# Kernel optimization log

Hardware: AMD Instinct MI355X
Metric: run time of the kernel (lower is better)

Reference implementation:

```python
import jax, jax.numpy as jnp
import numpy as np

D_MODEL = 1024
N_HEADS = 16
HEAD_DIM = D_MODEL // N_HEADS
N_MEM = 16
EPS = 1e-5
ROPE_THETA = 10000.0


def layernorm(x, g, b):
    mu = jnp.mean(x, axis=-1, keepdims=True)
    var = jnp.mean(jnp.square(x - mu), axis=-1, keepdims=True)
    return (x - mu) * jax.lax.rsqrt(var + EPS) * g + b


def rope_cos_sin(seq_len, head_dim, dtype):
    inv_freq = 1.0 / (ROPE_THETA ** (jnp.arange(0, head_dim, 2, dtype=jnp.float32) / head_dim))
    pos = jnp.arange(seq_len, dtype=jnp.float32)
    freqs = pos[:, None] * inv_freq[None, :]            # [S, hd/2]
    emb = jnp.concatenate([freqs, freqs], axis=-1)       # [S, hd]
    return jnp.cos(emb).astype(dtype), jnp.sin(emb).astype(dtype)


def rotate_half(x):
    x1, x2 = jnp.split(x, 2, axis=-1)
    return jnp.concatenate([-x2, x1], axis=-1)


def setup_inputs() -> dict:
    key = jax.random.key(0)
    ks = jax.random.split(key, 8)
    B, T, D = 2, 2048, D_MODEL
    x = jax.random.normal(ks[0], (B, T, D), dtype=jnp.float32)
    memory_tokens = jax.random.normal(ks[1], (1, N_MEM, D), dtype=jnp.float32) * 0.02
    s = 1.0 / np.sqrt(D)
    qkv_w = jax.random.uniform(ks[2], (3 * D, D), minval=-s, maxval=s, dtype=jnp.float32)
    qkv_b = jax.random.uniform(ks[3], (3 * D,), minval=-s, maxval=s, dtype=jnp.float32)
    out_w = jax.random.uniform(ks[4], (D, D), minval=-s, maxval=s, dtype=jnp.float32)
    out_b = jax.random.uniform(ks[5], (D,), minval=-s, maxval=s, dtype=jnp.float32)
    norm_g = jnp.ones((D,), jnp.float32)
    norm_b = jnp.zeros((D,), jnp.float32)
    normm_g = jnp.ones((D,), jnp.float32)
    normm_b = jnp.zeros((D,), jnp.float32)
    return {"x": x, "memory_tokens": memory_tokens, "qkv_w": qkv_w, "qkv_b": qkv_b,
            "out_w": out_w, "out_b": out_b, "norm_g": norm_g, "norm_b": norm_b,
            "normm_g": normm_g, "normm_b": normm_b}


def reference(x, memory_tokens, qkv_w, qkv_b, out_w, out_b, norm_g, norm_b, normm_g, normm_b):
    B, T, D = x.shape
    S = N_MEM + T
    residual = x
    x_norm = layernorm(x, norm_g, norm_b)
    mem = layernorm(jnp.broadcast_to(memory_tokens, (B, N_MEM, D)), normm_g, normm_b)
    xm = jnp.concatenate([mem, x_norm], axis=1)                # [B, S, D]
    qkv = xm @ qkv_w.T + qkv_b                                 # [B, S, 3D]
    qkv = qkv.reshape(B, S, 3, N_HEADS, HEAD_DIM)
    q = jnp.transpose(qkv[:, :, 0], (0, 2, 1, 3))              # [B, H, S, hd]
    k = jnp.transpose(qkv[:, :, 1], (0, 2, 1, 3))
    v = jnp.transpose(qkv[:, :, 2], (0, 2, 1, 3))
    cos, sin = rope_cos_sin(S, HEAD_DIM, x.dtype)              # [S, hd]
    q = q * cos + rotate_half(q) * sin
    k = k * cos + rotate_half(k) * sin
    scale = 1.0 / np.sqrt(HEAD_DIM)
    scores = jnp.einsum("bhqd,bhkd->bhqk", q, k) * scale       # [B, H, S, S]
    causal = jnp.tril(jnp.ones((S, S), dtype=bool))
    scores = jnp.where(causal, scores, jnp.finfo(scores.dtype).min)
    attn = jax.nn.softmax(scores, axis=-1)
    out = jnp.einsum("bhqk,bhkd->bhqd", attn, v)               # [B, H, S, hd]
    out = jnp.transpose(out, (0, 2, 1, 3)).reshape(B, S, D)
    out = out @ out_w.T + out_b
    out = out[:, N_MEM:, :]
    return residual + out
```

## Files before the change

### kernel.cpp

```cpp
#include <hip/hip_runtime.h>
#include <cstdint>


using bf16 = __bf16;
typedef __attribute__((ext_vector_type(8))) __bf16 bf16x8;
typedef __attribute__((ext_vector_type(4))) __bf16 bf16x4;
typedef __attribute__((ext_vector_type(4))) float floatx4;

#define MFMA16(a, b, c) __builtin_amdgcn_mfma_f32_16x16x32_bf16(a, b, c, 0, 0, 0)

constexpr int SV = 2064;
constexpr int SP = 2112;
constexpr float LOG2_THETA = 13.287712379549449f;

__device__ __forceinline__ bool dt_is_bf16(const void* p) {
  return *(const uint32_t*)p == 0x3F803F80u;
}

struct f8 { float v[8]; };

__device__ __forceinline__ f8 load8(const void* p, size_t idx, bool bf) {
  f8 r;
  if (bf) {
    bf16x8 t = *(const bf16x8*)((const bf16*)p + idx);
#pragma unroll
    for (int j = 0; j < 8; ++j) r.v[j] = (float)t[j];
  } else {
    float4 a = *(const float4*)((const float*)p + idx);
    float4 b = *(const float4*)((const float*)p + idx + 4);
    r.v[0] = a.x; r.v[1] = a.y; r.v[2] = a.z; r.v[3] = a.w;
    r.v[4] = b.x; r.v[5] = b.y; r.v[6] = b.z; r.v[7] = b.w;
  }
  return r;
}

__device__ __forceinline__ float ld1(const void* p, size_t idx, bool bf) {
  return bf ? (float)((const bf16*)p)[idx] : ((const float*)p)[idx];
}

__device__ __forceinline__ void load16_to_lds(const bf16* gptr, bf16* lptr) {
  auto* g = reinterpret_cast<const __attribute__((address_space(1))) uint32_t*>(
      reinterpret_cast<uintptr_t>(gptr));
  auto* l = reinterpret_cast<__attribute__((address_space(3))) uint32_t*>(
      reinterpret_cast<uintptr_t>(lptr));
  __builtin_amdgcn_global_load_lds(g, l, 16, 0, 0);
}

__device__ __forceinline__ unsigned cvtpk_bf16(float lo, float hi) {
  unsigned r;
  asm("v_cvt_pk_bf16_f32 %0, %1, %2" : "=v"(r) : "v"(lo), "v"(hi));
  return r;
}

__global__ __launch_bounds__(256) void conv_w(
    const void* __restrict__ W, const void* __restrict__ flagp,
    bf16* __restrict__ dst) {
  const bool bf = dt_is_bf16(flagp);
  const size_t i = ((size_t)blockIdx.x * 256 + threadIdx.x) * 8;
  const f8 v = load8(W, i, bf);
  bf16x8 o;
#pragma unroll
  for (int j = 0; j < 8; ++j) o[j] = (bf16)v.v[j];
  *(bf16x8*)&dst[i] = o;
}

__global__ __launch_bounds__(256) void rope_tab(float2* __restrict__ tab) {
  const int i = blockIdx.x * 256 + threadIdx.x;
  const int pos = i >> 5, f = i & 31;
  const float ang = (float)pos * exp2f((float)f * (-LOG2_THETA / 32.0f));
  float c, s;
  sincosf(ang, &c, &s);
  tab[i] = make_float2(c, s);
}

__global__ __launch_bounds__(256) void ln_all(
    const void* __restrict__ x, const void* __restrict__ mem,
    const void* __restrict__ ng, const void* __restrict__ nb,
    const void* __restrict__ mg, const void* __restrict__ mb,
    bf16* __restrict__ mem16, bf16* __restrict__ xln) {
  const bool bf = dt_is_bf16(ng);
  const int t = threadIdx.x, wid = t >> 6, lane = t & 63;
  const int row = blockIdx.x * 4 + wid;
  const void *src, *g, *bb;
  size_t soff;
  bf16* out;
  if (row < 16) {
    src = mem; soff = (size_t)row * 1024; g = mg; bb = mb;
    out = mem16 + (size_t)row * 1024;
  } else {
    src = x; soff = (size_t)(row - 16) * 1024; g = ng; bb = nb;
    out = xln + (size_t)(row - 16) * 1024;
  }
  const f8 v0 = load8(src, soff + lane * 8, bf);
  const f8 v1 = load8(src, soff + 512 + lane * 8, bf);
  float sum = 0.f, sq = 0.f;
#pragma unroll
  for (int j = 0; j < 8; ++j) { sum += v0.v[j]; sq += v0.v[j] * v0.v[j]; }
#pragma unroll
  for (int j = 0; j < 8; ++j) { sum += v1.v[j]; sq += v1.v[j] * v1.v[j]; }
#pragma unroll
  for (int off = 1; off < 64; off <<= 1) {
    sum += __shfl_xor(sum, off);
    sq += __shfl_xor(sq, off);
  }
  const float mu = sum * (1.0f / 1024.0f);
  const float var = sq * (1.0f / 1024.0f) - mu * mu;
  const float rstd = rsqrtf(var + 1e-5f);
  const f8 g0 = load8(g, lane * 8, bf), g1 = load8(g, 512 + lane * 8, bf);
  const f8 b0 = load8(bb, lane * 8, bf), b1 = load8(bb, 512 + lane * 8, bf);
  bf16x8 o0, o1;
#pragma unroll
  for (int j = 0; j < 8; ++j) {
    o0[j] = (bf16)((v0.v[j] - mu) * rstd * g0.v[j] + b0.v[j]);
    o1[j] = (bf16)((v1.v[j] - mu) * rstd * g1.v[j] + b1.v[j]);
  }
  *(bf16x8*)&out[lane * 8] = o0;
  *(bf16x8*)&out[512 + lane * 8] = o1;
}

__global__ __launch_bounds__(512, 1) void gemm0_rope(
    const bf16* __restrict__ mem16, const bf16* __restrict__ xln,
    const bf16* __restrict__ Wqb, const void* __restrict__ bias,
    const void* __restrict__ flagp, const float2* __restrict__ rtab,
    bf16* __restrict__ Qg, bf16* __restrict__ Kg, bf16* __restrict__ Vg) {
  const bool bf = dt_is_bf16(flagp);
  __shared__ bf16 SH[65536];
  const int t = threadIdx.x;
  const int row0 = blockIdx.x * 256;
  const int col0 = blockIdx.y * 256;
  const int wid = t >> 6, lane = t & 63, lr = lane & 15, lg = lane >> 4;
  const int wm = wid >> 2, wn = wid & 3;
  const int xorv = (lr & 7) << 3;

  const int coff = (((t & 7) ^ ((t >> 3) & 7)) << 3);
  const bf16* aptr[4];
  const bf16* bptr[4];
#pragma unroll
  for (int s = 0; s < 4; ++s) {
    int g = row0 + s * 64 + (t >> 3);
    if (g > 4127) g = 4127;
    const int b2 = (g >= SV) ? 1 : 0;
    const int ss = g - b2 * SV;
    const bf16* ap = (ss < 16) ? (mem16 + (size_t)ss * 1024)
                               : (xln + ((size_t)(b2 * 2048 + ss - 16)) * 1024);
    aptr[s] = ap + coff;
    bptr[s] = Wqb + (size_t)(col0 + s * 64 + (t >> 3)) * 1024 + coff;
  }

  const int ldsbase = (t & ~63) * 8;
  auto STAGE = [&](int bufi, int k0) {
    bf16* Ld = SH + bufi * 32768;
#pragma unroll
    for (int s = 0; s < 4; ++s)
      load16_to_lds(aptr[s] + k0, Ld + s * 4096 + ldsbase);
#pragma unroll
    for (int s = 0; s < 4; ++s)
      load16_to_lds(bptr[s] + k0, Ld + 16384 + s * 4096 + ldsbase);
  };

  floatx4 acc[8][4] = {};
  STAGE(0, 0);
  STAGE(1, 64);

  for (int kt = 0; kt < 16; ++kt) {
    const int cur = kt & 1;
    if (kt < 15)
      asm volatile("s_waitcnt vmcnt(8)" ::: "memory");
    else
      asm volatile("s_waitcnt vmcnt(0)" ::: "memory");
    __builtin_amdgcn_s_barrier();
    __builtin_amdgcn_sched_barrier(0);
    const bf16* Ab = SH + cur * 32768;
    const bf16* Bb = Ab + 16384;
    bf16x8 a0[8], b0[4], a1[8], b1[4];
#pragma unroll
    for (int mi = 0; mi < 8; ++mi)
      a0[mi] = *(const bf16x8*)&Ab[(wm * 128 + mi * 16 + lr) * 64 + ((lg * 8) ^ xorv)];
#pragma unroll
    for (int ni = 0; ni < 4; ++ni)
      b0[ni] = *(const bf16x8*)&Bb[(wn * 64 + ni * 16 + lr) * 64 + ((lg * 8) ^ xorv)];
    __builtin_amdgcn_s_setprio(1);
#pragma unroll
    for (int mi = 0; mi < 8; ++mi)
#pragma unroll
      for (int ni = 0; ni < 4; ++ni)
        acc[mi][ni] = MFMA16(a0[mi], b0[ni], acc[mi][ni]);
    __builtin_amdgcn_s_setprio(0);
#pragma unroll
    for (int mi = 0; mi < 8; ++mi)
      a1[mi] = *(const bf16x8*)&Ab[(wm * 128 + mi * 16 + lr) * 64 + ((32 + lg * 8) ^ xorv)];
#pragma unroll
    for (int ni = 0; ni < 4; ++ni)
      b1[ni] = *(const bf16x8*)&Bb[(wn * 64 + ni * 16 + lr) * 64 + ((32 + lg * 8) ^ xorv)];
    __builtin_amdgcn_sched_barrier(0);
    asm volatile("s_waitcnt lgkmcnt(0)" ::: "memory");
    __builtin_amdgcn_s_barrier();
    __builtin_amdgcn_sched_barrier(0);
    if (kt < 14) STAGE(cur, (kt + 2) * 64);
    __builtin_amdgcn_s_setprio(1);
#pragma unroll
    for (int mi = 0; mi < 8; ++mi)
#pragma unroll
      for (int ni = 0; ni < 4; ++ni)
        acc[mi][ni] = MFMA16(a1[mi], b1[ni], acc[mi][ni]);
    __builtin_amdgcn_s_setprio(0);
  }

  const int colbase = col0 + wn * 64;
  const int part = colbase >> 10;
  const int h = (colbase >> 6) & 15;
  const int row0w = row0 + wm * 128;

  if (part == 2) {
#pragma unroll
    for (int mi = 0; mi < 8; ++mi) {
      const int gq = row0w + mi * 16 + lg * 4;
      if (gq >= 2 * SV) continue;
      const int b2 = (gq >= SV) ? 1 : 0;
      const int pos = gq - b2 * SV;
      const size_t hb = (size_t)(b2 * 16 + h) * 64;
#pragma unroll
      for (int ni = 0; ni < 4; ++ni) {
        const int d = ni * 16 + lr;
        const float bc = ld1(bias, colbase + ni * 16 + lr, bf);
        bf16x4 vv;
#pragma unroll
        for (int r = 0; r < 4; ++r) vv[r] = (bf16)(acc[mi][ni][r] + bc);
        *(bf16x4*)&Vg[(hb + d) * SP + pos] = vv;
      }
    }
  } else {
    bf16* Dst = (part == 0) ? Qg : Kg;
    const float qs = (part == 0) ? 0.18033688011f : 1.0f;
    float bv[4];
#pragma unroll
    for (int a = 0; a < 4; ++a) bv[a] = ld1(bias, colbase + a * 16 + lr, bf);
#pragma unroll
    for (int mi = 0; mi < 8; ++mi) {
#pragma unroll
      for (int r = 0; r < 4; ++r) {
        const int g = row0w + mi * 16 + lg * 4 + r;
        if (g >= 2 * SV) continue;
        const int b2 = (g >= SV) ? 1 : 0;
        const int pos = g - b2 * SV;
        bf16* drow = Dst + ((size_t)(b2 * 16 + h) * SP + pos) * 64;
#pragma unroll
        for (int a = 0; a < 2; ++a) {
          const float2 cs = rtab[pos * 32 + a * 16 + lr];
          const float vlo = (acc[mi][a][r] + bv[a]) * qs;
          const float vhi = (acc[mi][a + 2][r] + bv[a + 2]) * qs;
          drow[a * 16 + lr] = (bf16)(vlo * cs.x - vhi * cs.y);
          drow[32 + a * 16 + lr] = (bf16)(vhi * cs.x + vlo * cs.y);
        }
      }
    }
  }
}

__global__ __launch_bounds__(256) void flash3(
    const bf16* __restrict__ Qg, const bf16* __restrict__ Kg,
    const bf16* __restrict__ Vg, bf16* __restrict__ attn_out) {
  const int qt = 32 - blockIdx.x;
  const int bh = blockIdx.y;
  const int b = bh >> 4, h = bh & 15;
  const bf16* Qb = Qg + (size_t)bh * SP * 64;
  const bf16* Kb = Kg + (size_t)bh * SP * 64;
  const bf16* Vb = Vg + (size_t)bh * 64 * SP;

  const int t = threadIdx.x;
  const int wid = t >> 6, lane = t & 63, lr = lane & 15, lg = lane >> 4;
  const int qw0 = qt * 64 + wid * 16;
  const int q = qw0 + lr;

  __shared__ bf16 Ks[2][64 * 72];
  __shared__ bf16 Vt[2][64 * 64];

  bf16x8 qf0{}, qf1{};
  if (q < SV) {
    qf0 = *(const bf16x8*)&Qb[(size_t)q * 64 + lg * 8];
    qf1 = *(const bf16x8*)&Qb[(size_t)q * 64 + 32 + lg * 8];
  }

  floatx4 o[4] = {};
  float lsum = 0.f;

  const int kr = t >> 2;
  const int kc = (t & 3) * 16;
  const int vd = t >> 2;
  const int vg0 = t & 3;
  const int vswz = ((vd & 7) ^ ((vd >> 4) & 3)) << 3;

  bf16x8 kA, kB, vA, vB;
  kA = *(const bf16x8*)&Kb[(size_t)kr * 64 + kc];
  kB = *(const bf16x8*)&Kb[(size_t)kr * 64 + kc + 8];
  vA = *(const bf16x8*)&Vb[(size_t)vd * SP + vg0 * 8];
  vB = *(const bf16x8*)&Vb[(size_t)vd * SP + (vg0 + 4) * 8];

  *(bf16x8*)&Ks[0][kr * 72 + kc] = kA;
  *(bf16x8*)&Ks[0][kr * 72 + kc + 8] = kB;
  *(bf16x8*)&Vt[0][vd * 64 + ((vg0 << 3) ^ vswz)] = vA;
  *(bf16x8*)&Vt[0][vd * 64 + (((vg0 + 4) << 3) ^ vswz)] = vB;
  if (qt >= 1) {
    kA = *(const bf16x8*)&Kb[(size_t)(64 + kr) * 64 + kc];
    kB = *(const bf16x8*)&Kb[(size_t)(64 + kr) * 64 + kc + 8];
    vA = *(const bf16x8*)&Vb[(size_t)vd * SP + 64 + vg0 * 8];
    vB = *(const bf16x8*)&Vb[(size_t)vd * SP + 64 + (vg0 + 4) * 8];
  }
  asm volatile("s_waitcnt lgkmcnt(0)" ::: "memory");
  __builtin_amdgcn_s_barrier();
  __builtin_amdgcn_sched_barrier(0);

  for (int kt = 0; kt <= qt; ++kt) {
    const int cur = kt & 1;
    const int k0 = kt * 64;
    if (kt < qt) {
      const int nb2 = cur ^ 1;
      *(bf16x8*)&Ks[nb2][kr * 72 + kc] = kA;
      *(bf16x8*)&Ks[nb2][kr * 72 + kc + 8] = kB;
      *(bf16x8*)&Vt[nb2][vd * 64 + ((vg0 << 3) ^ vswz)] = vA;
      *(bf16x8*)&Vt[nb2][vd * 64 + (((vg0 + 4) << 3) ^ vswz)] = vB;
      if (kt + 1 < qt) {
        const int kn = k0 + 128;
        kA = *(const bf16x8*)&Kb[(size_t)(kn + kr) * 64 + kc];
        kB = *(const bf16x8*)&Kb[(size_t)(kn + kr) * 64 + kc + 8];
        vA = *(const bf16x8*)&Vb[(size_t)vd * SP + kn + vg0 * 8];
        vB = *(const bf16x8*)&Vb[(size_t)vd * SP + kn + (vg0 + 4) * 8];
      }
    }

    floatx4 c[4] = {};
    __builtin_amdgcn_s_setprio(1);
#pragma unroll
    for (int j2 = 0; j2 < 4; ++j2) {
      const bf16x8 kfa = *(const bf16x8*)&Ks[cur][(j2 * 16 + lr) * 72 + lg * 8];
      const bf16x8 kfb = *(const bf16x8*)&Ks[cur][(j2 * 16 + lr) * 72 + 32 + lg * 8];
      c[j2] = MFMA16(kfa, qf0, c[j2]);
      c[j2] = MFMA16(kfb, qf1, c[j2]);
    }
    __builtin_amdgcn_s_setprio(0);

    const bool nm = (k0 + 63 > qw0);
    float pr[4][4];
#pragma unroll
    for (int j2 = 0; j2 < 4; ++j2) {
#pragma unroll
      for (int rr = 0; rr < 4; ++rr) {
        float s = c[j2][rr];
        if (nm && (k0 + j2 * 16 + lg * 4 + rr > q)) s = -1e30f;
        float p;
        asm("v_exp_f32 %0, %1" : "=v"(p) : "v"(s));
        lsum += p;
        pr[j2][rr] = p;
      }
    }

    unsigned paw[2][4];
#pragma unroll
    for (int cc = 0; cc < 2; ++cc) {
#pragma unroll
      for (int p_ = 0; p_ < 2; ++p_) {
        unsigned a = cvtpk_bf16(pr[2 * cc][2 * p_], pr[2 * cc][2 * p_ + 1]);
        unsigned b2 = cvtpk_bf16(pr[2 * cc + 1][2 * p_], pr[2 * cc + 1][2 * p_ + 1]);
        asm("v_permlane32_swap_b32 %0, %1" : "+v"(a), "+v"(b2));
        asm("v_permlane16_swap_b32 %0, %1" : "+v"(a), "+v"(b2));
        paw[cc][p_] = a;
        paw[cc][2 + p_] = b2;
      }
    }

    __builtin_amdgcn_s_setprio(1);
#pragma unroll
    for (int cc = 0; cc < 2; ++cc) {
      union { unsigned w[4]; bf16x8 v; } pu;
      pu.w[0] = paw[cc][0]; pu.w[1] = paw[cc][1];
      pu.w[2] = paw[cc][2]; pu.w[3] = paw[cc][3];
#pragma unroll
      for (int dt = 0; dt < 4; ++dt) {
        const int key8 = (cc * 32 + lg * 8) ^ ((((lr & 7) ^ dt)) << 3);
        const bf16x8 vf = *(const bf16x8*)&Vt[cur][(dt * 16 + lr) * 64 + key8];
        o[dt] = MFMA16(pu.v, vf, o[dt]);
      }
    }
    __builtin_amdgcn_s_setprio(0);
    asm volatile("s_waitcnt lgkmcnt(0)" ::: "memory");
    __builtin_amdgcn_s_barrier();
    __builtin_amdgcn_sched_barrier(0);
  }

  float l = lsum;
  l += __shfl_xor(l, 16);
  l += __shfl_xor(l, 32);
#pragma unroll
  for (int r = 0; r < 4; ++r) {
    const float lv = __shfl(l, lg * 4 + r);
    const int s = qw0 + lg * 4 + r;
    if (s < 16 || s >= SV) continue;
    const float inv = 1.0f / lv;
    const size_t rowoff = ((size_t)(b * 2048 + s - 16)) * 1024 + h * 64;
#pragma unroll
    for (int dt = 0; dt < 4; ++dt)
      attn_out[rowoff + dt * 16 + lr] = (bf16)(o[dt][r] * inv);
  }
}

__global__ __launch_bounds__(256) void gemm1_proj(
    const bf16* __restrict__ A, const bf16* __restrict__ Wob,
    const void* __restrict__ bias, const void* __restrict__ x,
    const void* __restrict__ flagp, void* __restrict__ outp) {
  const bool bf = dt_is_bf16(flagp);
  __shared__ bf16 As[128 * 32];
  __shared__ bf16 Bs[128 * 32];
  const int t = threadIdx.x;
  const int row0 = blockIdx.x * 128;
  const int col0 = blockIdx.y * 128;
  const int wid = t >> 6, lane = t & 63, lr = lane & 15, lg = lane >> 4;
  const int wrow = (wid >> 1) * 64, wcol = (wid & 1) * 64;
  floatx4 acc[4][4] = {};

  const bf16* agp[2];
  const bf16* bgp[2];
#pragma unroll
  for (int c = 0; c < 2; ++c) {
    const int tt = c * 256 + t;
    agp[c] = A + (size_t)(row0 + (tt >> 2)) * 1024 + (tt & 3) * 8;
    bgp[c] = Wob + (size_t)(col0 + (tt >> 2)) * 1024 + (tt & 3) * 8;
  }

  for (int k0 = 0; k0 < 1024; k0 += 32) {
    __syncthreads();
#pragma unroll
    for (int c = 0; c < 2; ++c) {
      const int tt = c * 256 + t;
      load16_to_lds(agp[c] + k0, &As[(tt & ~63) * 8]);
      load16_to_lds(bgp[c] + k0, &Bs[(tt & ~63) * 8]);
    }
    __syncthreads();
    bf16x8 af[4], bfr[4];
#pragma unroll
    for (int i = 0; i < 4; ++i) {
      af[i] = *(const bf16x8*)&As[(wrow + i * 16 + lr) * 32 + lg * 8];
      bfr[i] = *(const bf16x8*)&Bs[(wcol + i * 16 + lr) * 32 + lg * 8];
    }
#pragma unroll
    for (int mi = 0; mi < 4; ++mi)
#pragma unroll
      for (int ni = 0; ni < 4; ++ni)
        acc[mi][ni] = MFMA16(af[mi], bfr[ni], acc[mi][ni]);
  }

#pragma unroll
  for (int mi = 0; mi < 4; ++mi) {
#pragma unroll
    for (int r = 0; r < 4; ++r) {
      const int row = row0 + wrow + mi * 16 + lg * 4 + r;
#pragma unroll
      for (int ni = 0; ni < 4; ++ni) {
        const int col = col0 + wcol + ni * 16 + lr;
        const size_t idx = (size_t)row * 1024 + col;
        const float v = acc[mi][ni][r] + ld1(bias, col, bf) + ld1(x, idx, bf);
        if (bf)
          ((bf16*)outp)[idx] = (bf16)v;
        else
          ((float*)outp)[idx] = v;
      }
    }
  }
}

extern "C" void kernel_launch(void* const* d_in, const int* in_sizes, int n_in,
                              void* d_out, int out_size, void* d_ws, size_t ws_size,
                              hipStream_t stream) {
  const void* x = d_in[0];
  const void* mem = d_in[1];
  const void* qkvw = d_in[2];
  const void* qkvb = d_in[3];
  const void* outw = d_in[4];
  const void* outb = d_in[5];
  const void* ng = d_in[6];
  const void* nb = d_in[7];
  const void* mg = d_in[8];
  const void* mb = d_in[9];

  char* ws = (char*)d_ws;
  bf16* mem16 = (bf16*)(ws);
  bf16* xln = (bf16*)(ws + 32768);
  bf16* Qg = (bf16*)(ws + 8421376);
  bf16* Kg = (bf16*)(ws + 17072128);
  bf16* Vg = (bf16*)(ws + 25722880);
  bf16* Wqb = (bf16*)(ws + 34373632);
  bf16* Wob = (bf16*)(ws + 40665088);
  bf16* attn = xln;
  float2* rtab = (float2*)Wob;

  conv_w<<<1536, 256, 0, stream>>>(qkvw, ng, Wqb);
  ln_all<<<1028, 256, 0, stream>>>(x, mem, ng, nb, mg, mb, mem16, xln);
  rope_tab<<<258, 256, 0, stream>>>(rtab);
  gemm0_rope<<<dim3(17, 12), 512, 0, stream>>>(mem16, xln, Wqb, qkvb, ng, rtab,
                                               Qg, Kg, Vg);
  conv_w<<<512, 256, 0, stream>>>(outw, ng, Wob);
  flash3<<<dim3(33, 32), 256, 0, stream>>>(Qg, Kg, Vg, attn);
  gemm1_proj<<<dim3(32, 8), 256, 0, stream>>>(attn, Wob, outb, x, ng, d_out);
}
```

Baseline: 221.3 us.

## Double query rows per attention block and pipeline output projection GEMM

The attention kernel now gives each wave 32 query rows instead of 16, so each block covers 128 queries and each K/V tile loaded into LDS is reused across twice as many rows. Tiles entirely above the diagonal for a wave are skipped. The output projection GEMM moves to 512 threads with a 64-wide K step, double-buffered asynchronous LDS loads with swizzled layout, and split MFMA phases that overlap the next stage's loads. In exchange, register pressure rises in both kernels, the attention grid has half as many blocks, and causal load imbalance grows because each block is larger.

```diff
diff --git a/kernel.cpp b/kernel.cpp
--- a/kernel.cpp
+++ b/kernel.cpp
@@ -257,10 +257,40 @@
   }
 }
 
+__device__ __forceinline__ void softmax_pack(const floatx4* c, int qrow, int k0,
+                                             bool nm, int lg, float& lsum,
+                                             unsigned (&paw)[2][4]) {
+  float pr[4][4];
+#pragma unroll
+  for (int j2 = 0; j2 < 4; ++j2) {
+#pragma unroll
+    for (int rr = 0; rr < 4; ++rr) {
+      float s = c[j2][rr];
+      if (nm && (k0 + j2 * 16 + lg * 4 + rr > qrow)) s = -1e30f;
+      float p;
+      asm("v_exp_f32 %0, %1" : "=v"(p) : "v"(s));
+      lsum += p;
+      pr[j2][rr] = p;
+    }
+  }
+#pragma unroll
+  for (int cc = 0; cc < 2; ++cc) {
+#pragma unroll
+    for (int p_ = 0; p_ < 2; ++p_) {
+      unsigned a = cvtpk_bf16(pr[2 * cc][2 * p_], pr[2 * cc][2 * p_ + 1]);
+      unsigned b2 = cvtpk_bf16(pr[2 * cc + 1][2 * p_], pr[2 * cc + 1][2 * p_ + 1]);
+      asm("v_permlane32_swap_b32 %0, %1" : "+v"(a), "+v"(b2));
+      asm("v_permlane16_swap_b32 %0, %1" : "+v"(a), "+v"(b2));
+      paw[cc][p_] = a;
+      paw[cc][2 + p_] = b2;
+    }
+  }
+}
+
 __global__ __launch_bounds__(256) void flash3(
     const bf16* __restrict__ Qg, const bf16* __restrict__ Kg,
     const bf16* __restrict__ Vg, bf16* __restrict__ attn_out) {
-  const int qt = 32 - blockIdx.x;
+  const int st = 16 - blockIdx.x;
   const int bh = blockIdx.y;
   const int b = bh >> 4, h = bh & 15;
   const bf16* Qb = Qg + (size_t)bh * SP * 64;
@@ -269,20 +299,25 @@
 
   const int t = threadIdx.x;
   const int wid = t >> 6, lane = t & 63, lr = lane & 15, lg = lane >> 4;
-  const int qw0 = qt * 64 + wid * 16;
-  const int q = qw0 + lr;
+  const int qw0 = st * 128 + wid * 32;
+  const int q0 = qw0 + lr, q1 = q0 + 16;
+  const int nkt = min(2 * st + 2, 33);
 
   __shared__ bf16 Ks[2][64 * 72];
   __shared__ bf16 Vt[2][64 * 64];
 
-  bf16x8 qf0{}, qf1{};
-  if (q < SV) {
-    qf0 = *(const bf16x8*)&Qb[(size_t)q * 64 + lg * 8];
-    qf1 = *(const bf16x8*)&Qb[(size_t)q * 64 + 32 + lg * 8];
-  }
-
-  floatx4 o[4] = {};
-  float lsum = 0.f;
+  bf16x8 qf0a{}, qf0b{}, qf1a{}, qf1b{};
+  if (q0 < SV) {
+    qf0a = *(const bf16x8*)&Qb[(size_t)q0 * 64 + lg * 8];
+    qf0b = *(const bf16x8*)&Qb[(size_t)q0 * 64 + 32 + lg * 8];
+  }
+  if (q1 < SV) {
+    qf1a = *(const bf16x8*)&Qb[(size_t)q1 * 64 + lg * 8];
+    qf1b = *(const bf16x8*)&Qb[(size_t)q1 * 64 + 32 + lg * 8];
+  }
+
+  floatx4 o0[4] = {}, o1[4] = {};
+  float ls0 = 0.f, ls1 = 0.f;
 
   const int kr = t >> 2;
   const int kc = (t & 3) * 16;
@@ -300,26 +335,24 @@
   *(bf16x8*)&Ks[0][kr * 72 + kc + 8] = kB;
   *(bf16x8*)&Vt[0][vd * 64 + ((vg0 << 3) ^ vswz)] = vA;
   *(bf16x8*)&Vt[0][vd * 64 + (((vg0 + 4) << 3) ^ vswz)] = vB;
-  if (qt >= 1) {
-    kA = *(const bf16x8*)&Kb[(size_t)(64 + kr) * 64 + kc];
-    kB = *(const bf16x8*)&Kb[(size_t)(64 + kr) * 64 + kc + 8];
-    vA = *(const bf16x8*)&Vb[(size_t)vd * SP + 64 + vg0 * 8];
-    vB = *(const bf16x8*)&Vb[(size_t)vd * SP + 64 + (vg0 + 4) * 8];
-  }
+  kA = *(const bf16x8*)&Kb[(size_t)(64 + kr) * 64 + kc];
+  kB = *(const bf16x8*)&Kb[(size_t)(64 + kr) * 64 + kc + 8];
+  vA = *(const bf16x8*)&Vb[(size_t)vd * SP + 64 + vg0 * 8];
+  vB = *(const bf16x8*)&Vb[(size_t)vd * SP + 64 + (vg0 + 4) * 8];
   asm volatile("s_waitcnt lgkmcnt(0)" ::: "memory");
   __builtin_amdgcn_s_barrier();
   __builtin_amdgcn_sched_barrier(0);
 
-  for (int kt = 0; kt <= qt; ++kt) {
+  for (int kt = 0; kt < nkt; ++kt) {
     const int cur = kt & 1;
     const int k0 = kt * 64;
-    if (kt < qt) {
+    if (kt + 1 < nkt) {
       const int nb2 = cur ^ 1;
       *(bf16x8*)&Ks[nb2][kr * 72 + kc] = kA;
       *(bf16x8*)&Ks[nb2][kr * 72 + kc + 8] = kB;
       *(bf16x8*)&Vt[nb2][vd * 64 + ((vg0 << 3) ^ vswz)] = vA;
       *(bf16x8*)&Vt[nb2][vd * 64 + (((vg0 + 4) << 3) ^ vswz)] = vB;
-      if (kt + 1 < qt) {
+      if (kt + 2 < nkt) {
         const int kn = k0 + 128;
         kA = *(const bf16x8*)&Kb[(size_t)(kn + kr) * 64 + kc];
         kB = *(const bf16x8*)&Kb[(size_t)(kn + kr) * 64 + kc + 8];
@@ -328,134 +361,159 @@
       }
     }
 
-    floatx4 c[4] = {};
-    __builtin_amdgcn_s_setprio(1);
-#pragma unroll
-    for (int j2 = 0; j2 < 4; ++j2) {
-      const bf16x8 kfa = *(const bf16x8*)&Ks[cur][(j2 * 16 + lr) * 72 + lg * 8];
-      const bf16x8 kfb = *(const bf16x8*)&Ks[cur][(j2 * 16 + lr) * 72 + 32 + lg * 8];
-      c[j2] = MFMA16(kfa, qf0, c[j2]);
-      c[j2] = MFMA16(kfb, qf1, c[j2]);
-    }
-    __builtin_amdgcn_s_setprio(0);
-
-    const bool nm = (k0 + 63 > qw0);
-    float pr[4][4];
-#pragma unroll
-    for (int j2 = 0; j2 < 4; ++j2) {
-#pragma unroll
-      for (int rr = 0; rr < 4; ++rr) {
-        float s = c[j2][rr];
-        if (nm && (k0 + j2 * 16 + lg * 4 + rr > q)) s = -1e30f;
-        float p;
-        asm("v_exp_f32 %0, %1" : "=v"(p) : "v"(s));
-        lsum += p;
-        pr[j2][rr] = p;
+    if (k0 <= qw0 + 31) {
+      floatx4 c0[4] = {}, c1[4] = {};
+      __builtin_amdgcn_s_setprio(1);
+#pragma unroll
+      for (int j2 = 0; j2 < 4; ++j2) {
+        const bf16x8 kfa = *(const bf16x8*)&Ks[cur][(j2 * 16 + lr) * 72 + lg * 8];
+        const bf16x8 kfb = *(const bf16x8*)&Ks[cur][(j2 * 16 + lr) * 72 + 32 + lg * 8];
+        c0[j2] = MFMA16(kfa, qf0a, c0[j2]);
+        c0[j2] = MFMA16(kfb, qf0b, c0[j2]);
+        c1[j2] = MFMA16(kfa, qf1a, c1[j2]);
+        c1[j2] = MFMA16(kfb, qf1b, c1[j2]);
       }
-    }
-
-    unsigned paw[2][4];
-#pragma unroll
-    for (int cc = 0; cc < 2; ++cc) {
-#pragma unroll
-      for (int p_ = 0; p_ < 2; ++p_) {
-        unsigned a = cvtpk_bf16(pr[2 * cc][2 * p_], pr[2 * cc][2 * p_ + 1]);
-        unsigned b2 = cvtpk_bf16(pr[2 * cc + 1][2 * p_], pr[2 * cc + 1][2 * p_ + 1]);
-        asm("v_permlane32_swap_b32 %0, %1" : "+v"(a), "+v"(b2));
-        asm("v_permlane16_swap_b32 %0, %1" : "+v"(a), "+v"(b2));
-        paw[cc][p_] = a;
-        paw[cc][2 + p_] = b2;
+      __builtin_amdgcn_s_setprio(0);
+
+      unsigned paw0[2][4], paw1[2][4];
+      softmax_pack(c0, q0, k0, (k0 + 63 > qw0), lg, ls0, paw0);
+      softmax_pack(c1, q1, k0, (k0 + 63 > qw0 + 16), lg, ls1, paw1);
+
+      __builtin_amdgcn_s_setprio(1);
+#pragma unroll
+      for (int cc = 0; cc < 2; ++cc) {
+        union { unsigned w[4]; bf16x8 v; } pu0, pu1;
+#pragma unroll
+        for (int i = 0; i < 4; ++i) { pu0.w[i] = paw0[cc][i]; pu1.w[i] = paw1[cc][i]; }
+#pragma unroll
+        for (int dt = 0; dt < 4; ++dt) {
+          const int key8 = (cc * 32 + lg * 8) ^ ((((lr & 7) ^ dt)) << 3);
+          const bf16x8 vf = *(const bf16x8*)&Vt[cur][(dt * 16 + lr) * 64 + key8];
+          o0[dt] = MFMA16(pu0.v, vf, o0[dt]);
+          o1[dt] = MFMA16(pu1.v, vf, o1[dt]);
+        }
       }
-    }
-
-    __builtin_amdgcn_s_setprio(1);
-#pragma unroll
-    for (int cc = 0; cc < 2; ++cc) {
-      union { unsigned w[4]; bf16x8 v; } pu;
-      pu.w[0] = paw[cc][0]; pu.w[1] = paw[cc][1];
-      pu.w[2] = paw[cc][2]; pu.w[3] = paw[cc][3];
-#pragma unroll
-      for (int dt = 0; dt < 4; ++dt) {
-        const int key8 = (cc * 32 + lg * 8) ^ ((((lr & 7) ^ dt)) << 3);
-        const bf16x8 vf = *(const bf16x8*)&Vt[cur][(dt * 16 + lr) * 64 + key8];
-        o[dt] = MFMA16(pu.v, vf, o[dt]);
-      }
-    }
-    __builtin_amdgcn_s_setprio(0);
+      __builtin_amdgcn_s_setprio(0);
+    }
     asm volatile("s_waitcnt lgkmcnt(0)" ::: "memory");
     __builtin_amdgcn_s_barrier();
     __builtin_amdgcn_sched_barrier(0);
   }
 
-  float l = lsum;
-  l += __shfl_xor(l, 16);
-  l += __shfl_xor(l, 32);
+  float l0 = ls0, l1 = ls1;
+  l0 += __shfl_xor(l0, 16); l0 += __shfl_xor(l0, 32);
+  l1 += __shfl_xor(l1, 16); l1 += __shfl_xor(l1, 32);
 #pragma unroll
   for (int r = 0; r < 4; ++r) {
-    const float lv = __shfl(l, lg * 4 + r);
-    const int s = qw0 + lg * 4 + r;
-    if (s < 16 || s >= SV) continue;
-    const float inv = 1.0f / lv;
-    const size_t rowoff = ((size_t)(b * 2048 + s - 16)) * 1024 + h * 64;
-#pragma unroll
-    for (int dt = 0; dt < 4; ++dt)
-      attn_out[rowoff + dt * 16 + lr] = (bf16)(o[dt][r] * inv);
-  }
-}
-
-__global__ __launch_bounds__(256) void gemm1_proj(
+    const float lv0 = __shfl(l0, lg * 4 + r);
+    const float lv1 = __shfl(l1, lg * 4 + r);
+    const int s0 = qw0 + lg * 4 + r;
+    const int s1 = s0 + 16;
+    if (s0 >= 16 && s0 < SV) {
+      const float inv = 1.0f / lv0;
+      const size_t rowoff = ((size_t)(b * 2048 + s0 - 16)) * 1024 + h * 64;
+#pragma unroll
+      for (int dt = 0; dt < 4; ++dt)
+        attn_out[rowoff + dt * 16 + lr] = (bf16)(o0[dt][r] * inv);
+    }
+    if (s1 >= 16 && s1 < SV) {
+      const float inv = 1.0f / lv1;
+      const size_t rowoff = ((size_t)(b * 2048 + s1 - 16)) * 1024 + h * 64;
+#pragma unroll
+      for (int dt = 0; dt < 4; ++dt)
+        attn_out[rowoff + dt * 16 + lr] = (bf16)(o1[dt][r] * inv);
+    }
+  }
+}
+
+__global__ __launch_bounds__(512, 1) void gemm1_proj(
     const bf16* __restrict__ A, const bf16* __restrict__ Wob,
     const void* __restrict__ bias, const void* __restrict__ x,
     const void* __restrict__ flagp, void* __restrict__ outp) {
   const bool bf = dt_is_bf16(flagp);
-  __shared__ bf16 As[128 * 32];
-  __shared__ bf16 Bs[128 * 32];
+  __shared__ bf16 SH[32768];
   const int t = threadIdx.x;
   const int row0 = blockIdx.x * 128;
   const int col0 = blockIdx.y * 128;
   const int wid = t >> 6, lane = t & 63, lr = lane & 15, lg = lane >> 4;
-  const int wrow = (wid >> 1) * 64, wcol = (wid & 1) * 64;
-  floatx4 acc[4][4] = {};
-
-  const bf16* agp[2];
-  const bf16* bgp[2];
-#pragma unroll
-  for (int c = 0; c < 2; ++c) {
-    const int tt = c * 256 + t;
-    agp[c] = A + (size_t)(row0 + (tt >> 2)) * 1024 + (tt & 3) * 8;
-    bgp[c] = Wob + (size_t)(col0 + (tt >> 2)) * 1024 + (tt & 3) * 8;
-  }
-
-  for (int k0 = 0; k0 < 1024; k0 += 32) {
-    __syncthreads();
-#pragma unroll
-    for (int c = 0; c < 2; ++c) {
-      const int tt = c * 256 + t;
-      load16_to_lds(agp[c] + k0, &As[(tt & ~63) * 8]);
-      load16_to_lds(bgp[c] + k0, &Bs[(tt & ~63) * 8]);
-    }
-    __syncthreads();
-    bf16x8 af[4], bfr[4];
-#pragma unroll
-    for (int i = 0; i < 4; ++i) {
-      af[i] = *(const bf16x8*)&As[(wrow + i * 16 + lr) * 32 + lg * 8];
-      bfr[i] = *(const bf16x8*)&Bs[(wcol + i * 16 + lr) * 32 + lg * 8];
-    }
+  const int wm = wid >> 2, wn = wid & 3;
+  const int xorv = (lr & 7) << 3;
+
+  const int coff = (((t & 7) ^ ((t >> 3) & 7)) << 3);
+  const bf16* aptr[2];
+  const bf16* bptr[2];
+#pragma unroll
+  for (int s = 0; s < 2; ++s) {
+    aptr[s] = A + (size_t)(row0 + s * 64 + (t >> 3)) * 1024 + coff;
+    bptr[s] = Wob + (size_t)(col0 + s * 64 + (t >> 3)) * 1024 + coff;
+  }
+  const int ldsbase = (t & ~63) * 8;
+  auto STAGE = [&](int bufi, int k0) {
+    bf16* Ld = SH + bufi * 16384;
+#pragma unroll
+    for (int s = 0; s < 2; ++s)
+      load16_to_lds(aptr[s] + k0, Ld + s * 4096 + ldsbase);
+#pragma unroll
+    for (int s = 0; s < 2; ++s)
+      load16_to_lds(bptr[s] + k0, Ld + 8192 + s * 4096 + ldsbase);
+  };
+
+  floatx4 acc[4][2] = {};
+  STAGE(0, 0);
+  STAGE(1, 64);
+
+  for (int kt = 0; kt < 16; ++kt) {
+    const int cur = kt & 1;
+    if (kt < 15)
+      asm volatile("s_waitcnt vmcnt(4)" ::: "memory");
+    else
+      asm volatile("s_waitcnt vmcnt(0)" ::: "memory");
+    __builtin_amdgcn_s_barrier();
+    __builtin_amdgcn_sched_barrier(0);
+    const bf16* Ab = SH + cur * 16384;
+    const bf16* Bb = Ab + 8192;
+    bf16x8 a0[4], b0[2], a1[4], b1[2];
 #pragma unroll
     for (int mi = 0; mi < 4; ++mi)
-#pragma unroll
-      for (int ni = 0; ni < 4; ++ni)
-        acc[mi][ni] = MFMA16(af[mi], bfr[ni], acc[mi][ni]);
+      a0[mi] = *(const bf16x8*)&Ab[(wm * 64 + mi * 16 + lr) * 64 + ((lg * 8) ^ xorv)];
+#pragma unroll
+    for (int ni = 0; ni < 2; ++ni)
+      b0[ni] = *(const bf16x8*)&Bb[(wn * 32 + ni * 16 + lr) * 64 + ((lg * 8) ^ xorv)];
+    __builtin_amdgcn_s_setprio(1);
+#pragma unroll
+    for (int mi = 0; mi < 4; ++mi)
+#pragma unroll
+      for (int ni = 0; ni < 2; ++ni)
+        acc[mi][ni] = MFMA16(a0[mi], b0[ni], acc[mi][ni]);
+    __builtin_amdgcn_s_setprio(0);
+#pragma unroll
+    for (int mi = 0; mi < 4; ++mi)
+      a1[mi] = *(const bf16x8*)&Ab[(wm * 64 + mi * 16 + lr) * 64 + ((32 + lg * 8) ^ xorv)];
+#pragma unroll
+    for (int ni = 0; ni < 2; ++ni)
+      b1[ni] = *(const bf16x8*)&Bb[(wn * 32 + ni * 16 + lr) * 64 + ((32 + lg * 8) ^ xorv)];
+    __builtin_amdgcn_sched_barrier(0);
+    asm volatile("s_waitcnt lgkmcnt(0)" ::: "memory");
+    __builtin_amdgcn_s_barrier();
+    __builtin_amdgcn_sched_barrier(0);
+    if (kt < 14) STAGE(cur, (kt + 2) * 64);
+    __builtin_amdgcn_s_setprio(1);
+#pragma unroll
+    for (int mi = 0; mi < 4; ++mi)
+#pragma unroll
+      for (int ni = 0; ni < 2; ++ni)
+        acc[mi][ni] = MFMA16(a1[mi], b1[ni], acc[mi][ni]);
+    __builtin_amdgcn_s_setprio(0);
   }
 
 #pragma unroll
   for (int mi = 0; mi < 4; ++mi) {
 #pragma unroll
     for (int r = 0; r < 4; ++r) {
-      const int row = row0 + wrow + mi * 16 + lg * 4 + r;
-#pragma unroll
-      for (int ni = 0; ni < 4; ++ni) {
-        const int col = col0 + wcol + ni * 16 + lr;
+      const int row = row0 + wm * 64 + mi * 16 + lg * 4 + r;
+#pragma unroll
+      for (int ni = 0; ni < 2; ++ni) {
+        const int col = col0 + wn * 32 + ni * 16 + lr;
         const size_t idx = (size_t)row * 1024 + col;
         const float v = acc[mi][ni][r] + ld1(bias, col, bf) + ld1(x, idx, bf);
         if (bf)
@@ -498,6 +556,6 @@
   gemm0_rope<<<dim3(17, 12), 512, 0, stream>>>(mem16, xln, Wqb, qkvb, ng, rtab,
                                                Qg, Kg, Vg);
   conv_w<<<512, 256, 0, stream>>>(outw, ng, Wob);
-  flash3<<<dim3(33, 32), 256, 0, stream>>>(Qg, Kg, Vg, attn);
-  gemm1_proj<<<dim3(32, 8), 256, 0, stream>>>(attn, Wob, outb, x, ng, d_out);
-}
+  flash3<<<dim3(17, 32), 256, 0, stream>>>(Qg, Kg, Vg, attn);
+  gemm1_proj<<<dim3(32, 8), 512, 0, stream>>>(attn, Wob, outb, x, ng, d_out);
+}
```

After: 228.6 us. +3.3%, slower.
